# Kernel optimization log

Measured on AMD Instinct MI355X. Metric: run time of the kernel, lower is better.

Reference implementation:

```python
import jax, jax.numpy as jnp
import numpy as np

B, S, D = 2, 2048, 1024
H = 16
HD = D // H


def setup_inputs() -> dict:
    key = jax.random.key(0)
    ks = jax.random.split(key, 6)
    X = jax.random.normal(ks[0], (B, S, D), dtype=jnp.float32)
    # Linear weights stored [in, out] so y = x @ W (torch stores transposed).
    sc = 1.0 / np.sqrt(D)
    Wq = jax.random.normal(ks[1], (D, D), dtype=jnp.float32) * sc
    Wk = jax.random.normal(ks[2], (D, D), dtype=jnp.float32) * sc
    Wv = jax.random.normal(ks[3], (D, D), dtype=jnp.float32) * sc
    Wo = jax.random.normal(ks[4], (D, D), dtype=jnp.float32) * sc
    bo = jax.random.normal(ks[5], (D,), dtype=jnp.float32) * 0.01
    return {"X": X, "Wq": Wq, "Wk": Wk, "Wv": Wv, "Wo": Wo, "bo": bo}


def reference(X, Wq, Wk, Wv, Wo, bo):
    b, n, _ = X.shape
    # QKV projections (no bias, qkv_bias=False), reshape to [b, h, n, hd]
    q = (X @ Wq).reshape(b, n, H, HD).transpose(0, 2, 1, 3)
    k = (X @ Wk).reshape(b, n, H, HD).transpose(0, 2, 1, 3)
    v = (X @ Wv).reshape(b, n, H, HD).transpose(0, 2, 1, 3)
    # Unscaled scores (module's scale flag defaults to False)
    scores = jnp.einsum("bhqd,bhkd->bhqk", q, k)
    causal = jnp.triu(jnp.ones((n, n), dtype=bool), k=1)  # True above diagonal
    scores = jnp.where(causal, -jnp.inf, scores)
    attn = jax.nn.softmax(scores, axis=-1)
    # dropout p=0.0 -> identity
    ctx = jnp.einsum("bhqk,bhkd->bqhd", attn, v).reshape(b, n, H * HD)
    return ctx @ Wo + bo
```

## Files before the change

### kernel.cpp

```cpp
#include <hip/hip_runtime.h>
#include <stdint.h>


typedef __attribute__((ext_vector_type(8))) short short8;
typedef __attribute__((ext_vector_type(4))) float floatx4;

#define S_LEN 2048
#define D_DIM 1024
#define NH 16
#define HD 64
#define L2E 1.44269504088896340736f

__device__ __forceinline__ short f2bf(float f) {
    uint32_t u = __builtin_bit_cast(uint32_t, f);
    uint32_t r = u + 0x7fffu + ((u >> 16) & 1u);
    return (short)(r >> 16);
}
__device__ __forceinline__ uint32_t pack2(float a, float b) {
#if __has_builtin(__builtin_amdgcn_cvt_pk_bf16_f32)
    auto v = __builtin_amdgcn_cvt_pk_bf16_f32(a, b);
    uint32_t r; __builtin_memcpy(&r, &v, sizeof(r)); return r;
#else
    return (uint32_t)(uint16_t)f2bf(a) | ((uint32_t)(uint16_t)f2bf(b) << 16);
#endif
}
__device__ __forceinline__ void gll16(const void* g, void* l) {
    __builtin_amdgcn_global_load_lds(
        (const __attribute__((address_space(1))) void*)g,
        (__attribute__((address_space(3))) void*)l, 16, 0, 0);
}

__global__ __launch_bounds__(256) void prep_kernel(const float* __restrict__ X,
                                                   const float* __restrict__ Wq,
                                                   const float* __restrict__ Wk,
                                                   const float* __restrict__ Wv,
                                                   const float* __restrict__ Wo,
                                                   short* __restrict__ Xb,
                                                   short* __restrict__ WqkvT,
                                                   short* __restrict__ WoT) {
    const int b = blockIdx.x, tid = threadIdx.x;
    if (b < 4096) {
        const int i = b * 256 + tid;
        const float4 v = *(const float4*)(X + (size_t)i * 4);
        uint2 o;
        o.x = pack2(v.x, v.y);
        o.y = pack2(v.z, v.w);
        *(uint2*)(Xb + (size_t)i * 4) = o;
    } else {
        const int b2 = b - 4096;
        const int z = b2 >> 10, w = b2 & 1023;
        const float* W = (z == 0) ? Wq : (z == 1) ? Wk : (z == 2) ? Wv : Wo;
        short* WT = (z < 3) ? (WqkvT + (size_t)z * 1024 * 1024) : WoT;
        __shared__ float tile[32][33];
        const int bx = (w & 31) * 32;
        const int by = (w >> 5) * 32;
        const int tx = tid & 31, ty = tid >> 5;
        for (int i = 0; i < 32; i += 8)
            tile[ty + i][tx] = W[(size_t)(bx + ty + i) * D_DIM + by + tx];
        __syncthreads();
        for (int i = 0; i < 32; i += 8)
            WT[(size_t)(by + ty + i) * D_DIM + bx + tx] = f2bf(tile[tx][ty + i]);
    }
}

__global__ __launch_bounds__(256, 3) void gemm_qkv_kernel(const short* __restrict__ Xb,
                                                          const short* __restrict__ WT,
                                                          short* __restrict__ Qb,
                                                          short* __restrict__ Kb,
                                                          short* __restrict__ Vtb) {
    __shared__ __align__(16) short smem[16384];
    short (*As)[4096] = (short(*)[4096])smem;
    short (*Bs)[4096] = (short(*)[4096])(smem + 8192);
    const int m0 = blockIdx.x * 128, n0 = blockIdx.y * 128;
    const int tid = threadIdx.x, lane = tid & 63, wave = tid >> 6;
    const int ln = lane & 15, quad = lane >> 4;
    const int mw = (wave & 1) * 64, nw = (wave >> 1) * 64;
    floatx4 acc[4][4] = {};

    const int c0 = tid, c1 = 256 + tid;
    const int r0 = c0 >> 2, s0 = (c0 & 3) ^ ((r0 >> 1) & 3);
    const int r1 = c1 >> 2, s1 = (c1 & 3) ^ ((r1 >> 1) & 3);
    const short* A0 = Xb + (size_t)(m0 + r0) * D_DIM + s0 * 8;
    const short* A1 = Xb + (size_t)(m0 + r1) * D_DIM + s1 * 8;
    const short* B0 = WT + (size_t)(n0 + r0) * D_DIM + s0 * 8;
    const short* B1 = WT + (size_t)(n0 + r1) * D_DIM + s1 * 8;

#define QSTAGE(buf, kk)                                    \
    {                                                      \
        const int o = (kk) * 32;                           \
        gll16(A0 + o, &As[buf][c0 * 8]);                   \
        gll16(A1 + o, &As[buf][c1 * 8]);                   \
        gll16(B0 + o, &Bs[buf][c0 * 8]);                   \
        gll16(B1 + o, &Bs[buf][c1 * 8]);                   \
    }

    QSTAGE(0, 0);
    int cur = 0;
    for (int kk = 0; kk < 32; kk++) {
        if (kk + 1 < 32) {
            QSTAGE(cur ^ 1, kk + 1);
            asm volatile("s_waitcnt vmcnt(4)" ::: "memory");
        } else {
            asm volatile("s_waitcnt vmcnt(0)" ::: "memory");
        }
        __builtin_amdgcn_s_barrier();
        __builtin_amdgcn_sched_barrier(0);
        short8 a[4], b[4];
        for (int i = 0; i < 4; i++) {
            const int row = mw + i * 16 + ln;
            a[i] = *(const short8*)(&As[cur][row * 32 + ((quad ^ ((row >> 1) & 3)) * 8)]);
        }
        for (int j = 0; j < 4; j++) {
            const int row = nw + j * 16 + ln;
            b[j] = *(const short8*)(&Bs[cur][row * 32 + ((quad ^ ((row >> 1) & 3)) * 8)]);
        }
        __builtin_amdgcn_s_setprio(1);
        for (int i = 0; i < 4; i++)
            for (int j = 0; j < 4; j++)
                acc[i][j] = __builtin_amdgcn_mfma_f32_16x16x32_bf16(a[i], b[j], acc[i][j], 0, 0, 0);
        __builtin_amdgcn_s_setprio(0);
        __builtin_amdgcn_sched_barrier(0);
        __builtin_amdgcn_s_barrier();
        __builtin_amdgcn_sched_barrier(0);
        cur ^= 1;
    }
#undef QSTAGE

    const int nsel = n0 >> 10;
    if (nsel < 2) {
        const float qs = (nsel == 0) ? L2E : 1.f;
        short* outB = (nsel == 0) ? Qb : Kb;
        for (int i = 0; i < 4; i++)
            for (int j = 0; j < 4; j++)
                for (int r = 0; r < 4; r++) {
                    const int row = m0 + mw + i * 16 + quad * 4 + r;
                    const int col = (n0 & 1023) + nw + j * 16 + ln;
                    const int bb = row >> 11, s = row & (S_LEN - 1);
                    const int h = col >> 6, hd = col & (HD - 1);
                    outB[(((size_t)(bb * NH + h)) * S_LEN + s) * HD + hd] = f2bf(acc[i][j][r] * qs);
                }
    } else {
        for (int i = 0; i < 4; i++)
            for (int j = 0; j < 4; j++) {
                const int feat = nw + j * 16 + ln;
                const int tok  = mw + i * 16 + quad * 4;
                const int t8 = tok >> 3, lo = tok & 7;
                uint2 u;
                u.x = pack2(acc[i][j][0], acc[i][j][1]);
                u.y = pack2(acc[i][j][2], acc[i][j][3]);
                *(uint2*)&smem[feat * 128 + ((t8 ^ (feat & 15)) * 8) + lo] = u;
            }
        __syncthreads();
        const int bb = m0 >> 11, sbase = m0 & (S_LEN - 1);
        for (int c = tid; c < 2048; c += 256) {
            const int feat = c >> 4, t8 = c & 15;
            const short8 v = *(const short8*)&smem[feat * 128 + ((t8 ^ (feat & 15)) * 8)];
            const int col = (n0 & 1023) + feat;
            const int h = col >> 6, hd = col & (HD - 1);
            const int s = sbase + t8 * 8;
            *(short8*)(Vtb + (((size_t)(bb * NH + h)) * HD + hd) * S_LEN + s) = v;
        }
    }
}

__global__ __launch_bounds__(256, 3) void gemm_out_kernel(const short* __restrict__ Cb,
                                                          const short* __restrict__ WoT,
                                                          float* __restrict__ out,
                                                          const float* __restrict__ bias) {
    __shared__ __align__(16) short As[2][128 * 32];
    __shared__ __align__(16) short Bs[2][64 * 32];
    const int m0 = blockIdx.x * 128, n0 = blockIdx.y * 64;
    const int tid = threadIdx.x, lane = tid & 63;
    const int ln = lane & 15, quad = lane >> 4;
    const int wave = tid >> 6;
    const int mw = (wave & 1) * 64, nw = (wave >> 1) * 32;

    floatx4 acc[4][2] = {};

    const int c0 = tid, c1 = 256 + tid;
    const int r0 = c0 >> 2, s0 = (c0 & 3) ^ ((r0 >> 1) & 3);
    const int r1 = c1 >> 2, s1 = (c1 & 3) ^ ((r1 >> 1) & 3);
    const short* A0 = Cb + (size_t)(m0 + r0) * D_DIM + s0 * 8;
    const short* A1 = Cb + (size_t)(m0 + r1) * D_DIM + s1 * 8;
    const short* B0 = WoT + (size_t)(n0 + r0) * D_DIM + s0 * 8;

#define OSTAGE(buf, kk)                                    \
    {                                                      \
        const int o = (kk) * 32;                           \
        gll16(A0 + o, &As[buf][c0 * 8]);                   \
        gll16(A1 + o, &As[buf][c1 * 8]);                   \
        gll16(B0 + o, &Bs[buf][c0 * 8]);                   \
    }

    OSTAGE(0, 0);
    int cur = 0;
    for (int kk = 0; kk < 32; kk++) {
        if (kk + 1 < 32) {
            OSTAGE(cur ^ 1, kk + 1);
            asm volatile("s_waitcnt vmcnt(3)" ::: "memory");
        } else {
            asm volatile("s_waitcnt vmcnt(0)" ::: "memory");
        }
        __builtin_amdgcn_s_barrier();
        __builtin_amdgcn_sched_barrier(0);
        short8 a[4], b[2];
        for (int i = 0; i < 4; i++) {
            const int row = mw + i * 16 + ln;
            a[i] = *(const short8*)(&As[cur][row * 32 + ((quad ^ ((row >> 1) & 3)) * 8)]);
        }
        for (int j = 0; j < 2; j++) {
            const int row = nw + j * 16 + ln;
            b[j] = *(const short8*)(&Bs[cur][row * 32 + ((quad ^ ((row >> 1) & 3)) * 8)]);
        }
        __builtin_amdgcn_s_setprio(1);
        for (int i = 0; i < 4; i++)
            for (int j = 0; j < 2; j++)
                acc[i][j] = __builtin_amdgcn_mfma_f32_16x16x32_bf16(a[i], b[j], acc[i][j], 0, 0, 0);
        __builtin_amdgcn_s_setprio(0);
        __builtin_amdgcn_sched_barrier(0);
        __builtin_amdgcn_s_barrier();
        __builtin_amdgcn_sched_barrier(0);
        cur ^= 1;
    }
#undef OSTAGE

    for (int i = 0; i < 4; i++)
        for (int j = 0; j < 2; j++)
            for (int r = 0; r < 4; r++) {
                const int row = m0 + mw + i * 16 + quad * 4 + r;
                const int col = n0 + nw + j * 16 + ln;
                out[(size_t)row * D_DIM + col] = acc[i][j][r] + bias[col];
            }
}

__global__ __launch_bounds__(512, 6) void attn_kernel(const short* __restrict__ Q,
                                                      const short* __restrict__ Kg,
                                                      const short* __restrict__ Vt,
                                                      short* __restrict__ ctx,
                                                      float* __restrict__ Opart,
                                                      float* __restrict__ Lpart,
                                                      int bh_base) {
    __shared__ __align__(16) short Ks[2][64 * 64];
    __shared__ __align__(16) short Vs[2][64 * 64];
    __shared__ __align__(16) short Ps[8][640];

    const int tid = threadIdx.x, wave = tid >> 6, lane = tid & 63;
    const int ln = lane & 15, quad = lane >> 4;

    const int id = blockIdx.x;
    const int bh = bh_base + (id & 7) + 8 * ((id >> 3) & 1);
    const int t = id >> 4;

    static const unsigned char TASK[24] = {
        0xF0, 0xE1, 0xD0, 0xC1, 0xB0, 0xA1, 0x90, 0x81,
        0xF1, 0xE0, 0xD1, 0xC0, 0xB1, 0xA0, 0x91, 0x80,
        0x02, 0x12, 0x22, 0x32, 0x42, 0x52, 0x62, 0x72};
    const int code = TASK[t];
    const int qt = code >> 4, mode = code & 3;
    const int n = qt + 1, h0 = n >> 1;
    const int kb = 2 * ((mode == 1) ? h0 : 0);
    const int ke = 2 * ((mode == 0) ? h0 : n);
    const int pidx   = (mode == 2) ? -1 : ((qt - 8) * 32 + bh) * 2 + mode;
    const int kmask0 = 2 * qt;
    const int q0 = qt * 128;
    const int bb = bh >> 4, h = bh & 15;
    short* Pw = Ps[wave];

    const short* qrow = Q + ((size_t)bh * S_LEN + q0 + wave * 16 + ln) * HD;
    const short8 qb0 = *(const short8*)(qrow + quad * 8);
    const short8 qb1 = *(const short8*)(qrow + 32 + quad * 8);
    const int q_abs = q0 + wave * 16 + ln;

    const int srow = tid >> 3, spos = tid & 7, ssrc = spos ^ (srow & 7);
    const size_t kbase = (size_t)bh * S_LEN * HD;
    const size_t vbase = (size_t)bh * HD * S_LEN;

    float l_part = 0.f;
    floatx4 o_acc[4] = {};

#define STAGE(buf, kt_)                                                          \
    {                                                                            \
        const int k0s = (kt_) * 64;                                              \
        gll16(Kg + kbase + (size_t)(k0s + srow) * HD + ssrc * 8,                 \
              &Ks[buf][tid * 8]);                                                \
        gll16(Vt + vbase + (size_t)srow * S_LEN + k0s + ssrc * 8,                \
              &Vs[buf][tid * 8]);                                                \
    }

    int cur = 0;
    STAGE(0, kb);
    for (int kt = kb; kt < ke; kt++) {
        if (kt + 1 < ke) {
            STAGE(cur ^ 1, kt + 1);
            asm volatile("s_waitcnt vmcnt(2)" ::: "memory");
        } else {
            asm volatile("s_waitcnt vmcnt(0)" ::: "memory");
        }
        __builtin_amdgcn_s_barrier();
        __builtin_amdgcn_sched_barrier(0);

        const short* Kc = Ks[cur];
        const short* Vc = Vs[cur];

        floatx4 sc4[4];
        __builtin_amdgcn_s_setprio(1);
        for (int nt = 0; nt < 4; nt++) {
            const int row = nt * 16 + ln;
            const short8 ak0 = *(const short8*)(Kc + row * 64 + ((quad ^ (ln & 7)) * 8));
            const short8 ak1 = *(const short8*)(Kc + row * 64 + (((4 + quad) ^ (ln & 7)) * 8));
            floatx4 z = {};
            z = __builtin_amdgcn_mfma_f32_16x16x32_bf16(ak0, qb0, z, 0, 0, 0);
            z = __builtin_amdgcn_mfma_f32_16x16x32_bf16(ak1, qb1, z, 0, 0, 0);
            sc4[nt] = z;
        }
        __builtin_amdgcn_s_setprio(0);

        if (kt >= kmask0) {
            const int k0 = kt * 64;
            for (int nt = 0; nt < 4; nt++)
                for (int r = 0; r < 4; r++)
                    if (k0 + nt * 16 + quad * 4 + r > q_abs) sc4[nt][r] = -1e30f;
        }

        float ls = 0.f;
        for (int nt = 0; nt < 4; nt++)
            for (int r = 0; r < 4; r++) {
                const float e = exp2f(sc4[nt][r]);
                sc4[nt][r] = e; ls += e;
            }
        l_part += ls;

        for (int p = 0; p < 2; p++) {
            uint2 u0, u1;
            u0.x = pack2(sc4[2 * p][0], sc4[2 * p][1]);
            u0.y = pack2(sc4[2 * p][2], sc4[2 * p][3]);
            u1.x = pack2(sc4[2 * p + 1][0], sc4[2 * p + 1][1]);
            u1.y = pack2(sc4[2 * p + 1][2], sc4[2 * p + 1][3]);
            *(uint2*)&Pw[ln * 40 + quad * 4]      = u0;
            *(uint2*)&Pw[ln * 40 + 16 + quad * 4] = u1;
            const short8 bp = *(const short8*)&Pw[ln * 40 + quad * 8];
            __builtin_amdgcn_s_setprio(1);
            for (int dt = 0; dt < 4; dt++) {
                const int row = dt * 16 + ln;
                const short8 av = *(const short8*)(Vc + row * 64 + (((p * 4 + quad) ^ (ln & 7)) * 8));
                o_acc[dt] = __builtin_amdgcn_mfma_f32_16x16x32_bf16(av, bp, o_acc[dt], 0, 0, 0);
            }
            __builtin_amdgcn_s_setprio(0);
        }

        __builtin_amdgcn_sched_barrier(0);
        __builtin_amdgcn_s_barrier();
        __builtin_amdgcn_sched_barrier(0);
        cur ^= 1;
    }
#undef STAGE

    float l_tot = l_part;
    l_tot += __shfl_xor(l_tot, 16, 64);
    l_tot += __shfl_xor(l_tot, 32, 64);

    if (pidx >= 0) {
        float* Ob = Opart + (size_t)pidx * 8192 + (wave * 16 + ln) * 64;
        for (int dt = 0; dt < 4; dt++)
            *(float4*)(Ob + dt * 16 + quad * 4) = *(float4*)&o_acc[dt];
        if (quad == 0) Lpart[(size_t)pidx * 128 + wave * 16 + ln] = l_tot;
    } else {
        const float rl = 1.f / l_tot;
        const int qr = lane >> 2, sg = lane & 3;
        for (int c = 0; c < 2; c++) {
            for (int dd = 0; dd < 2; dd++) {
                const int dt = c * 2 + dd;
                uint2 u;
                u.x = pack2(o_acc[dt][0] * rl, o_acc[dt][1] * rl);
                u.y = pack2(o_acc[dt][2] * rl, o_acc[dt][3] * rl);
                *(uint2*)&Pw[ln * 40 + dd * 16 + quad * 4] = u;
            }
            const short8 v = *(const short8*)&Pw[qr * 40 + sg * 8];
            const int s = q0 + wave * 16 + qr;
            *(short8*)(ctx + ((size_t)bb * S_LEN + s) * D_DIM + h * HD + sg * 8 + c * 32) = v;
        }
    }
}

__global__ __launch_bounds__(256) void combine_kernel(const float* __restrict__ Opart,
                                                      const float* __restrict__ Lpart,
                                                      short* __restrict__ ctx) {
    const int tile = blockIdx.x;
    const int qt = 8 + (tile >> 5), bh = tile & 31;
    const int bb = bh >> 4, h = bh & 15;
    const int p0 = ((qt - 8) * 32 + bh) * 2;
    const float* O0 = Opart + (size_t)p0 * 8192;
    const float* O1 = O0 + 8192;
    const float* l0 = Lpart + (size_t)p0 * 128;
    const float* l1 = l0 + 128;
    for (int e = threadIdx.x; e < 2048; e += 256) {
        const int q = e >> 4, seg = e & 15;
        const float rl = 1.f / (l0[q] + l1[q]);
        const float4 x0 = *(const float4*)(O0 + q * 64 + seg * 4);
        const float4 x1 = *(const float4*)(O1 + q * 64 + seg * 4);
        uint2 u;
        u.x = pack2((x0.x + x1.x) * rl, (x0.y + x1.y) * rl);
        u.y = pack2((x0.z + x1.z) * rl, (x0.w + x1.w) * rl);
        const int s = qt * 128 + q;
        *(uint2*)(ctx + ((size_t)bb * S_LEN + s) * D_DIM + h * HD + seg * 4) = u;
    }
}

extern "C" void kernel_launch(void* const* d_in, const int* in_sizes, int n_in,
                              void* d_out, int out_size, void* d_ws, size_t ws_size,
                              hipStream_t stream) {
    const float* X  = (const float*)d_in[0];
    const float* Wq = (const float*)d_in[1];
    const float* Wk = (const float*)d_in[2];
    const float* Wv = (const float*)d_in[3];
    const float* Wo = (const float*)d_in[4];
    const float* bo = (const float*)d_in[5];
    float* out = (float*)d_out;

    char* ws = (char*)d_ws;
    const size_t MB = 1024 * 1024;
    short* Xb     = (short*)(ws);
    short* WqkvT  = (short*)(ws + 8  * MB);
    short* Qb     = (short*)(ws + 16 * MB);
    short* Kb     = (short*)(ws + 24 * MB);
    short* Vtb    = (short*)(ws + 32 * MB);
    short* ctxb   = (short*)(ws + 40 * MB);
    short* WoT    = (short*)(ws + 48 * MB);
    float* Opart  = (float*)(ws);
    float* Lpart  = (float*)(ws + 50 * MB);

    prep_kernel<<<8192, 256, 0, stream>>>(X, Wq, Wk, Wv, Wo, Xb, WqkvT, WoT);

    dim3 gq(32, 24);
    gemm_qkv_kernel<<<gq, 256, 0, stream>>>(Xb, WqkvT, Qb, Kb, Vtb);

    attn_kernel<<<384, 512, 0, stream>>>(Qb, Kb, Vtb, ctxb, Opart, Lpart, 0);
    attn_kernel<<<384, 512, 0, stream>>>(Qb, Kb, Vtb, ctxb, Opart, Lpart, 16);
    combine_kernel<<<256, 256, 0, stream>>>(Opart, Lpart, ctxb);

    dim3 go(32, 16);
    gemm_out_kernel<<<go, 256, 0, stream>>>(ctxb, WoT, out, bo);
}
```

Baseline: 204.8 us.

## Drop split-K attention and combine kernel; use 128-wide KV tiles in one launch

Replaces the two split-KV attention launches and the fp32 partial-combine kernel with a single launch of 512 blocks. Each block handles one query tile over its full causal KV range and orders blocks longest-first to balance load. KV tiles grow from 64 to 128 keys, halving the loop iterations and barriers, at the cost of twice the LDS, more registers and a lower occupancy hint (6 to 4). It also removes the partial-result global traffic and one kernel launch, but long query tiles can no longer be split across blocks, so the tail may be less balanced.

Result: faster. 178.8 us (-12.7%).

```diff
diff --git a/kernel.cpp b/kernel.cpp
--- a/kernel.cpp
+++ b/kernel.cpp
@@ -233,35 +233,22 @@
             }
 }
 
-__global__ __launch_bounds__(512, 6) void attn_kernel(const short* __restrict__ Q,
+__global__ __launch_bounds__(512, 4) void attn_kernel(const short* __restrict__ Q,
                                                       const short* __restrict__ Kg,
                                                       const short* __restrict__ Vt,
-                                                      short* __restrict__ ctx,
-                                                      float* __restrict__ Opart,
-                                                      float* __restrict__ Lpart,
-                                                      int bh_base) {
-    __shared__ __align__(16) short Ks[2][64 * 64];
-    __shared__ __align__(16) short Vs[2][64 * 64];
+                                                      short* __restrict__ ctx) {
+    __shared__ __align__(16) short Ks[2][128 * 64];
+    __shared__ __align__(16) short Vs[2][64 * 128];
     __shared__ __align__(16) short Ps[8][640];
 
     const int tid = threadIdx.x, wave = tid >> 6, lane = tid & 63;
     const int ln = lane & 15, quad = lane >> 4;
 
     const int id = blockIdx.x;
-    const int bh = bh_base + (id & 7) + 8 * ((id >> 3) & 1);
-    const int t = id >> 4;
-
-    static const unsigned char TASK[24] = {
-        0xF0, 0xE1, 0xD0, 0xC1, 0xB0, 0xA1, 0x90, 0x81,
-        0xF1, 0xE0, 0xD1, 0xC0, 0xB1, 0xA0, 0x91, 0x80,
-        0x02, 0x12, 0x22, 0x32, 0x42, 0x52, 0x62, 0x72};
-    const int code = TASK[t];
-    const int qt = code >> 4, mode = code & 3;
-    const int n = qt + 1, h0 = n >> 1;
-    const int kb = 2 * ((mode == 1) ? h0 : 0);
-    const int ke = 2 * ((mode == 0) ? h0 : n);
-    const int pidx   = (mode == 2) ? -1 : ((qt - 8) * 32 + bh) * 2 + mode;
-    const int kmask0 = 2 * qt;
+    const int hv = (id < 256) ? id : id - 256;
+    const int bh = (hv & 7) + 8 * ((hv >> 3) & 3);
+    const int qt = (id < 256) ? 8 + (hv >> 5) : 7 - (hv >> 5);
+    const int ke = qt + 1;
     const int q0 = qt * 128;
     const int bb = bh >> 4, h = bh & 15;
     short* Pw = Ps[wave];
@@ -271,28 +258,32 @@
     const short8 qb1 = *(const short8*)(qrow + 32 + quad * 8);
     const int q_abs = q0 + wave * 16 + ln;
 
-    const int srow = tid >> 3, spos = tid & 7, ssrc = spos ^ (srow & 7);
     const size_t kbase = (size_t)bh * S_LEN * HD;
     const size_t vbase = (size_t)bh * HD * S_LEN;
+    const int ck0 = tid, ck1 = tid + 512;
+    const int kr0 = ck0 >> 3, ks0 = (ck0 & 7) ^ (kr0 & 7);
+    const int kr1 = ck1 >> 3, ks1 = (ck1 & 7) ^ (kr1 & 7);
+    const int vr0 = ck0 >> 4, vs0 = (ck0 & 15) ^ (vr0 & 15);
+    const int vr1 = ck1 >> 4, vs1 = (ck1 & 15) ^ (vr1 & 15);
 
     float l_part = 0.f;
     floatx4 o_acc[4] = {};
 
-#define STAGE(buf, kt_)                                                          \
-    {                                                                            \
-        const int k0s = (kt_) * 64;                                              \
-        gll16(Kg + kbase + (size_t)(k0s + srow) * HD + ssrc * 8,                 \
-              &Ks[buf][tid * 8]);                                                \
-        gll16(Vt + vbase + (size_t)srow * S_LEN + k0s + ssrc * 8,                \
-              &Vs[buf][tid * 8]);                                                \
+#define STAGE(buf, kt_)                                                           \
+    {                                                                             \
+        const int k0s = (kt_) * 128;                                              \
+        gll16(Kg + kbase + (size_t)(k0s + kr0) * HD + ks0 * 8, &Ks[buf][ck0 * 8]);\
+        gll16(Kg + kbase + (size_t)(k0s + kr1) * HD + ks1 * 8, &Ks[buf][ck1 * 8]);\
+        gll16(Vt + vbase + (size_t)vr0 * S_LEN + k0s + vs0 * 8, &Vs[buf][ck0 * 8]);\
+        gll16(Vt + vbase + (size_t)vr1 * S_LEN + k0s + vs1 * 8, &Vs[buf][ck1 * 8]);\
     }
 
     int cur = 0;
-    STAGE(0, kb);
-    for (int kt = kb; kt < ke; kt++) {
+    STAGE(0, 0);
+    for (int kt = 0; kt < ke; kt++) {
         if (kt + 1 < ke) {
             STAGE(cur ^ 1, kt + 1);
-            asm volatile("s_waitcnt vmcnt(2)" ::: "memory");
+            asm volatile("s_waitcnt vmcnt(4)" ::: "memory");
         } else {
             asm volatile("s_waitcnt vmcnt(0)" ::: "memory");
         }
@@ -302,47 +293,47 @@
         const short* Kc = Ks[cur];
         const short* Vc = Vs[cur];
 
-        floatx4 sc4[4];
+        floatx4 sc[8];
         __builtin_amdgcn_s_setprio(1);
-        for (int nt = 0; nt < 4; nt++) {
+        for (int nt = 0; nt < 8; nt++) {
             const int row = nt * 16 + ln;
             const short8 ak0 = *(const short8*)(Kc + row * 64 + ((quad ^ (ln & 7)) * 8));
             const short8 ak1 = *(const short8*)(Kc + row * 64 + (((4 + quad) ^ (ln & 7)) * 8));
             floatx4 z = {};
             z = __builtin_amdgcn_mfma_f32_16x16x32_bf16(ak0, qb0, z, 0, 0, 0);
             z = __builtin_amdgcn_mfma_f32_16x16x32_bf16(ak1, qb1, z, 0, 0, 0);
-            sc4[nt] = z;
+            sc[nt] = z;
         }
         __builtin_amdgcn_s_setprio(0);
 
-        if (kt >= kmask0) {
-            const int k0 = kt * 64;
-            for (int nt = 0; nt < 4; nt++)
+        if (kt == qt) {
+            const int k0 = kt * 128;
+            for (int nt = 0; nt < 8; nt++)
                 for (int r = 0; r < 4; r++)
-                    if (k0 + nt * 16 + quad * 4 + r > q_abs) sc4[nt][r] = -1e30f;
+                    if (k0 + nt * 16 + quad * 4 + r > q_abs) sc[nt][r] = -1e30f;
         }
 
         float ls = 0.f;
-        for (int nt = 0; nt < 4; nt++)
+        for (int nt = 0; nt < 8; nt++)
             for (int r = 0; r < 4; r++) {
-                const float e = exp2f(sc4[nt][r]);
-                sc4[nt][r] = e; ls += e;
+                const float e = exp2f(sc[nt][r]);
+                sc[nt][r] = e; ls += e;
             }
         l_part += ls;
 
-        for (int p = 0; p < 2; p++) {
+        for (int p = 0; p < 4; p++) {
             uint2 u0, u1;
-            u0.x = pack2(sc4[2 * p][0], sc4[2 * p][1]);
-            u0.y = pack2(sc4[2 * p][2], sc4[2 * p][3]);
-            u1.x = pack2(sc4[2 * p + 1][0], sc4[2 * p + 1][1]);
-            u1.y = pack2(sc4[2 * p + 1][2], sc4[2 * p + 1][3]);
+            u0.x = pack2(sc[2 * p][0], sc[2 * p][1]);
+            u0.y = pack2(sc[2 * p][2], sc[2 * p][3]);
+            u1.x = pack2(sc[2 * p + 1][0], sc[2 * p + 1][1]);
+            u1.y = pack2(sc[2 * p + 1][2], sc[2 * p + 1][3]);
             *(uint2*)&Pw[ln * 40 + quad * 4]      = u0;
             *(uint2*)&Pw[ln * 40 + 16 + quad * 4] = u1;
             const short8 bp = *(const short8*)&Pw[ln * 40 + quad * 8];
             __builtin_amdgcn_s_setprio(1);
             for (int dt = 0; dt < 4; dt++) {
                 const int row = dt * 16 + ln;
-                const short8 av = *(const short8*)(Vc + row * 64 + (((p * 4 + quad) ^ (ln & 7)) * 8));
+                const short8 av = *(const short8*)(Vc + row * 128 + (((p * 4 + quad) ^ (ln & 15)) * 8));
                 o_acc[dt] = __builtin_amdgcn_mfma_f32_16x16x32_bf16(av, bp, o_acc[dt], 0, 0, 0);
             }
             __builtin_amdgcn_s_setprio(0);
@@ -359,50 +350,19 @@
     l_tot += __shfl_xor(l_tot, 16, 64);
     l_tot += __shfl_xor(l_tot, 32, 64);
 
-    if (pidx >= 0) {
-        float* Ob = Opart + (size_t)pidx * 8192 + (wave * 16 + ln) * 64;
-        for (int dt = 0; dt < 4; dt++)
-            *(float4*)(Ob + dt * 16 + quad * 4) = *(float4*)&o_acc[dt];
-        if (quad == 0) Lpart[(size_t)pidx * 128 + wave * 16 + ln] = l_tot;
-    } else {
-        const float rl = 1.f / l_tot;
-        const int qr = lane >> 2, sg = lane & 3;
-        for (int c = 0; c < 2; c++) {
-            for (int dd = 0; dd < 2; dd++) {
-                const int dt = c * 2 + dd;
-                uint2 u;
-                u.x = pack2(o_acc[dt][0] * rl, o_acc[dt][1] * rl);
-                u.y = pack2(o_acc[dt][2] * rl, o_acc[dt][3] * rl);
-                *(uint2*)&Pw[ln * 40 + dd * 16 + quad * 4] = u;
-            }
-            const short8 v = *(const short8*)&Pw[qr * 40 + sg * 8];
-            const int s = q0 + wave * 16 + qr;
-            *(short8*)(ctx + ((size_t)bb * S_LEN + s) * D_DIM + h * HD + sg * 8 + c * 32) = v;
-        }
-    }
-}
-
-__global__ __launch_bounds__(256) void combine_kernel(const float* __restrict__ Opart,
-                                                      const float* __restrict__ Lpart,
-                                                      short* __restrict__ ctx) {
-    const int tile = blockIdx.x;
-    const int qt = 8 + (tile >> 5), bh = tile & 31;
-    const int bb = bh >> 4, h = bh & 15;
-    const int p0 = ((qt - 8) * 32 + bh) * 2;
-    const float* O0 = Opart + (size_t)p0 * 8192;
-    const float* O1 = O0 + 8192;
-    const float* l0 = Lpart + (size_t)p0 * 128;
-    const float* l1 = l0 + 128;
-    for (int e = threadIdx.x; e < 2048; e += 256) {
-        const int q = e >> 4, seg = e & 15;
-        const float rl = 1.f / (l0[q] + l1[q]);
-        const float4 x0 = *(const float4*)(O0 + q * 64 + seg * 4);
-        const float4 x1 = *(const float4*)(O1 + q * 64 + seg * 4);
-        uint2 u;
-        u.x = pack2((x0.x + x1.x) * rl, (x0.y + x1.y) * rl);
-        u.y = pack2((x0.z + x1.z) * rl, (x0.w + x1.w) * rl);
-        const int s = qt * 128 + q;
-        *(uint2*)(ctx + ((size_t)bb * S_LEN + s) * D_DIM + h * HD + seg * 4) = u;
+    const float rl = 1.f / l_tot;
+    const int qr = lane >> 2, sg = lane & 3;
+    for (int c = 0; c < 2; c++) {
+        for (int dd = 0; dd < 2; dd++) {
+            const int dt = c * 2 + dd;
+            uint2 u;
+            u.x = pack2(o_acc[dt][0] * rl, o_acc[dt][1] * rl);
+            u.y = pack2(o_acc[dt][2] * rl, o_acc[dt][3] * rl);
+            *(uint2*)&Pw[ln * 40 + dd * 16 + quad * 4] = u;
+        }
+        const short8 v = *(const short8*)&Pw[qr * 40 + sg * 8];
+        const int s = q0 + wave * 16 + qr;
+        *(short8*)(ctx + ((size_t)bb * S_LEN + s) * D_DIM + h * HD + sg * 8 + c * 32) = v;
     }
 }
 
@@ -426,17 +386,13 @@
     short* Vtb    = (short*)(ws + 32 * MB);
     short* ctxb   = (short*)(ws + 40 * MB);
     short* WoT    = (short*)(ws + 48 * MB);
-    float* Opart  = (float*)(ws);
-    float* Lpart  = (float*)(ws + 50 * MB);
 
     prep_kernel<<<8192, 256, 0, stream>>>(X, Wq, Wk, Wv, Wo, Xb, WqkvT, WoT);
 
     dim3 gq(32, 24);
     gemm_qkv_kernel<<<gq, 256, 0, stream>>>(Xb, WqkvT, Qb, Kb, Vtb);
 
-    attn_kernel<<<384, 512, 0, stream>>>(Qb, Kb, Vtb, ctxb, Opart, Lpart, 0);
-    attn_kernel<<<384, 512, 0, stream>>>(Qb, Kb, Vtb, ctxb, Opart, Lpart, 16);
-    combine_kernel<<<256, 256, 0, stream>>>(Opart, Lpart, ctxb);
+    attn_kernel<<<512, 512, 0, stream>>>(Qb, Kb, Vtb, ctxb);
 
     dim3 go(32, 16);
     gemm_out_kernel<<<go, 256, 0, stream>>>(ctxb, WoT, out, bo);
```

## Replace split-KV static attention schedule with persistent atomic work queue

Applied to the files above, without the earlier changes.

Removes the static split-KV task table, the partial-output buffers and the combine kernel. One persistent attention launch now pulls (q-tile, head) tasks in longest-first order from a global atomic counter, which prep_kernel resets. This drops a launch and the partial-sum round trip through memory, and balances the causal triangle's uneven work dynamically. In exchange, each long q-tile is done by a single block with no KV split, and every task pays for an atomic fetch plus an extra barrier.

Result: no change. 203.3 us (-0.8%).

```diff
diff --git a/kernel.cpp b/kernel.cpp
--- a/kernel.cpp
+++ b/kernel.cpp
@@ -37,9 +37,11 @@
                                                    const float* __restrict__ Wo,
                                                    short* __restrict__ Xb,
                                                    short* __restrict__ WqkvT,
-                                                   short* __restrict__ WoT) {
+                                                   short* __restrict__ WoT,
+                                                   int* __restrict__ ctr) {
     const int b = blockIdx.x, tid = threadIdx.x;
     if (b < 4096) {
+        if (b == 0 && tid == 0) ctr[0] = 0;
         const int i = b * 256 + tid;
         const float4 v = *(const float4*)(X + (size_t)i * 4);
         uint2 o;
@@ -237,46 +239,42 @@
                                                       const short* __restrict__ Kg,
                                                       const short* __restrict__ Vt,
                                                       short* __restrict__ ctx,
-                                                      float* __restrict__ Opart,
-                                                      float* __restrict__ Lpart,
-                                                      int bh_base) {
+                                                      int* __restrict__ ctr) {
     __shared__ __align__(16) short Ks[2][64 * 64];
     __shared__ __align__(16) short Vs[2][64 * 64];
     __shared__ __align__(16) short Ps[8][640];
+    __shared__ int s_task;
 
     const int tid = threadIdx.x, wave = tid >> 6, lane = tid & 63;
     const int ln = lane & 15, quad = lane >> 4;
-
-    const int id = blockIdx.x;
-    const int bh = bh_base + (id & 7) + 8 * ((id >> 3) & 1);
-    const int t = id >> 4;
-
-    static const unsigned char TASK[24] = {
-        0xF0, 0xE1, 0xD0, 0xC1, 0xB0, 0xA1, 0x90, 0x81,
-        0xF1, 0xE0, 0xD1, 0xC0, 0xB1, 0xA0, 0x91, 0x80,
-        0x02, 0x12, 0x22, 0x32, 0x42, 0x52, 0x62, 0x72};
-    const int code = TASK[t];
-    const int qt = code >> 4, mode = code & 3;
-    const int n = qt + 1, h0 = n >> 1;
-    const int kb = 2 * ((mode == 1) ? h0 : 0);
-    const int ke = 2 * ((mode == 0) ? h0 : n);
-    const int pidx   = (mode == 2) ? -1 : ((qt - 8) * 32 + bh) * 2 + mode;
-    const int kmask0 = 2 * qt;
-    const int q0 = qt * 128;
-    const int bb = bh >> 4, h = bh & 15;
     short* Pw = Ps[wave];
 
-    const short* qrow = Q + ((size_t)bh * S_LEN + q0 + wave * 16 + ln) * HD;
-    const short8 qb0 = *(const short8*)(qrow + quad * 8);
-    const short8 qb1 = *(const short8*)(qrow + 32 + quad * 8);
-    const int q_abs = q0 + wave * 16 + ln;
-
     const int srow = tid >> 3, spos = tid & 7, ssrc = spos ^ (srow & 7);
-    const size_t kbase = (size_t)bh * S_LEN * HD;
-    const size_t vbase = (size_t)bh * HD * S_LEN;
-
-    float l_part = 0.f;
-    floatx4 o_acc[4] = {};
+
+    for (;;) {
+        if (tid == 0) s_task = atomicAdd(ctr, 1);
+        __syncthreads();
+        const int t = s_task;
+        if (t >= 512) return;
+
+        const int qt = 15 - (t >> 5);
+        const int hv = t & 31;
+        const int bh = (hv & 7) + 8 * ((hv >> 3) & 3);
+        const int ke = 2 * (qt + 1);
+        const int kmask0 = 2 * qt;
+        const int q0 = qt * 128;
+        const int bb = bh >> 4, h = bh & 15;
+
+        const short* qrow = Q + ((size_t)bh * S_LEN + q0 + wave * 16 + ln) * HD;
+        const short8 qb0 = *(const short8*)(qrow + quad * 8);
+        const short8 qb1 = *(const short8*)(qrow + 32 + quad * 8);
+        const int q_abs = q0 + wave * 16 + ln;
+
+        const size_t kbase = (size_t)bh * S_LEN * HD;
+        const size_t vbase = (size_t)bh * HD * S_LEN;
+
+        float l_part = 0.f;
+        floatx4 o_acc[4] = {};
 
 #define STAGE(buf, kt_)                                                          \
     {                                                                            \
@@ -287,84 +285,78 @@
               &Vs[buf][tid * 8]);                                                \
     }
 
-    int cur = 0;
-    STAGE(0, kb);
-    for (int kt = kb; kt < ke; kt++) {
-        if (kt + 1 < ke) {
-            STAGE(cur ^ 1, kt + 1);
-            asm volatile("s_waitcnt vmcnt(2)" ::: "memory");
-        } else {
-            asm volatile("s_waitcnt vmcnt(0)" ::: "memory");
-        }
-        __builtin_amdgcn_s_barrier();
-        __builtin_amdgcn_sched_barrier(0);
-
-        const short* Kc = Ks[cur];
-        const short* Vc = Vs[cur];
-
-        floatx4 sc4[4];
-        __builtin_amdgcn_s_setprio(1);
-        for (int nt = 0; nt < 4; nt++) {
-            const int row = nt * 16 + ln;
-            const short8 ak0 = *(const short8*)(Kc + row * 64 + ((quad ^ (ln & 7)) * 8));
-            const short8 ak1 = *(const short8*)(Kc + row * 64 + (((4 + quad) ^ (ln & 7)) * 8));
-            floatx4 z = {};
-            z = __builtin_amdgcn_mfma_f32_16x16x32_bf16(ak0, qb0, z, 0, 0, 0);
-            z = __builtin_amdgcn_mfma_f32_16x16x32_bf16(ak1, qb1, z, 0, 0, 0);
-            sc4[nt] = z;
-        }
-        __builtin_amdgcn_s_setprio(0);
-
-        if (kt >= kmask0) {
-            const int k0 = kt * 64;
+        int cur = 0;
+        STAGE(0, 0);
+        for (int kt = 0; kt < ke; kt++) {
+            if (kt + 1 < ke) {
+                STAGE(cur ^ 1, kt + 1);
+                asm volatile("s_waitcnt vmcnt(2)" ::: "memory");
+            } else {
+                asm volatile("s_waitcnt vmcnt(0)" ::: "memory");
+            }
+            __builtin_amdgcn_s_barrier();
+            __builtin_amdgcn_sched_barrier(0);
+
+            const short* Kc = Ks[cur];
+            const short* Vc = Vs[cur];
+
+            floatx4 sc4[4];
+            __builtin_amdgcn_s_setprio(1);
+            for (int nt = 0; nt < 4; nt++) {
+                const int row = nt * 16 + ln;
+                const short8 ak0 = *(const short8*)(Kc + row * 64 + ((quad ^ (ln & 7)) * 8));
+                const short8 ak1 = *(const short8*)(Kc + row * 64 + (((4 + quad) ^ (ln & 7)) * 8));
+                floatx4 z = {};
+                z = __builtin_amdgcn_mfma_f32_16x16x32_bf16(ak0, qb0, z, 0, 0, 0);
+                z = __builtin_amdgcn_mfma_f32_16x16x32_bf16(ak1, qb1, z, 0, 0, 0);
+                sc4[nt] = z;
+            }
+            __builtin_amdgcn_s_setprio(0);
+
+            if (kt >= kmask0) {
+                const int k0 = kt * 64;
+                for (int nt = 0; nt < 4; nt++)
+                    for (int r = 0; r < 4; r++)
+                        if (k0 + nt * 16 + quad * 4 + r > q_abs) sc4[nt][r] = -1e30f;
+            }
+
+            float ls = 0.f;
             for (int nt = 0; nt < 4; nt++)
-                for (int r = 0; r < 4; r++)
-                    if (k0 + nt * 16 + quad * 4 + r > q_abs) sc4[nt][r] = -1e30f;
-        }
-
-        float ls = 0.f;
-        for (int nt = 0; nt < 4; nt++)
-            for (int r = 0; r < 4; r++) {
-                const float e = exp2f(sc4[nt][r]);
-                sc4[nt][r] = e; ls += e;
-            }
-        l_part += ls;
-
-        for (int p = 0; p < 2; p++) {
-            uint2 u0, u1;
-            u0.x = pack2(sc4[2 * p][0], sc4[2 * p][1]);
-            u0.y = pack2(sc4[2 * p][2], sc4[2 * p][3]);
-            u1.x = pack2(sc4[2 * p + 1][0], sc4[2 * p + 1][1]);
-            u1.y = pack2(sc4[2 * p + 1][2], sc4[2 * p + 1][3]);
-            *(uint2*)&Pw[ln * 40 + quad * 4]      = u0;
-            *(uint2*)&Pw[ln * 40 + 16 + quad * 4] = u1;
-            const short8 bp = *(const short8*)&Pw[ln * 40 + quad * 8];
-            __builtin_amdgcn_s_setprio(1);
-            for (int dt = 0; dt < 4; dt++) {
-                const int row = dt * 16 + ln;
-                const short8 av = *(const short8*)(Vc + row * 64 + (((p * 4 + quad) ^ (ln & 7)) * 8));
-                o_acc[dt] = __builtin_amdgcn_mfma_f32_16x16x32_bf16(av, bp, o_acc[dt], 0, 0, 0);
-            }
-            __builtin_amdgcn_s_setprio(0);
-        }
-
-        __builtin_amdgcn_sched_barrier(0);
-        __builtin_amdgcn_s_barrier();
-        __builtin_amdgcn_sched_barrier(0);
-        cur ^= 1;
-    }
+                for (int r = 0; r < 4; r++) {
+                    const float e = exp2f(sc4[nt][r]);
+                    sc4[nt][r] = e; ls += e;
+                }
+            l_part += ls;
+
+            for (int p = 0; p < 2; p++) {
+                uint2 u0, u1;
+                u0.x = pack2(sc4[2 * p][0], sc4[2 * p][1]);
+                u0.y = pack2(sc4[2 * p][2], sc4[2 * p][3]);
+                u1.x = pack2(sc4[2 * p + 1][0], sc4[2 * p + 1][1]);
+                u1.y = pack2(sc4[2 * p + 1][2], sc4[2 * p + 1][3]);
+                *(uint2*)&Pw[ln * 40 + quad * 4]      = u0;
+                *(uint2*)&Pw[ln * 40 + 16 + quad * 4] = u1;
+                const short8 bp = *(const short8*)&Pw[ln * 40 + quad * 8];
+                __builtin_amdgcn_s_setprio(1);
+                for (int dt = 0; dt < 4; dt++) {
+                    const int row = dt * 16 + ln;
+                    const short8 av = *(const short8*)(Vc + row * 64 + (((p * 4 + quad) ^ (ln & 7)) * 8));
+                    o_acc[dt] = __builtin_amdgcn_mfma_f32_16x16x32_bf16(av, bp, o_acc[dt], 0, 0, 0);
+                }
+                __builtin_amdgcn_s_setprio(0);
+            }
+
+            __builtin_amdgcn_sched_barrier(0);
+            __builtin_amdgcn_s_barrier();
+            __builtin_amdgcn_sched_barrier(0);
+            cur ^= 1;
+        }
 #undef STAGE
 
-    float l_tot = l_part;
-    l_tot += __shfl_xor(l_tot, 16, 64);
-    l_tot += __shfl_xor(l_tot, 32, 64);
-
-    if (pidx >= 0) {
-        float* Ob = Opart + (size_t)pidx * 8192 + (wave * 16 + ln) * 64;
-        for (int dt = 0; dt < 4; dt++)
-            *(float4*)(Ob + dt * 16 + quad * 4) = *(float4*)&o_acc[dt];
-        if (quad == 0) Lpart[(size_t)pidx * 128 + wave * 16 + ln] = l_tot;
-    } else {
+        float l_tot = l_part;
+        l_tot += __shfl_xor(l_tot, 16, 64);
+        l_tot += __shfl_xor(l_tot, 32, 64);
+
         const float rl = 1.f / l_tot;
         const int qr = lane >> 2, sg = lane & 3;
         for (int c = 0; c < 2; c++) {
@@ -379,30 +371,7 @@
             const int s = q0 + wave * 16 + qr;
             *(short8*)(ctx + ((size_t)bb * S_LEN + s) * D_DIM + h * HD + sg * 8 + c * 32) = v;
         }
-    }
-}
-
-__global__ __launch_bounds__(256) void combine_kernel(const float* __restrict__ Opart,
-                                                      const float* __restrict__ Lpart,
-                                                      short* __restrict__ ctx) {
-    const int tile = blockIdx.x;
-    const int qt = 8 + (tile >> 5), bh = tile & 31;
-    const int bb = bh >> 4, h = bh & 15;
-    const int p0 = ((qt - 8) * 32 + bh) * 2;
-    const float* O0 = Opart + (size_t)p0 * 8192;
-    const float* O1 = O0 + 8192;
-    const float* l0 = Lpart + (size_t)p0 * 128;
-    const float* l1 = l0 + 128;
-    for (int e = threadIdx.x; e < 2048; e += 256) {
-        const int q = e >> 4, seg = e & 15;
-        const float rl = 1.f / (l0[q] + l1[q]);
-        const float4 x0 = *(const float4*)(O0 + q * 64 + seg * 4);
-        const float4 x1 = *(const float4*)(O1 + q * 64 + seg * 4);
-        uint2 u;
-        u.x = pack2((x0.x + x1.x) * rl, (x0.y + x1.y) * rl);
-        u.y = pack2((x0.z + x1.z) * rl, (x0.w + x1.w) * rl);
-        const int s = qt * 128 + q;
-        *(uint2*)(ctx + ((size_t)bb * S_LEN + s) * D_DIM + h * HD + seg * 4) = u;
+        __syncthreads();
     }
 }
 
@@ -426,17 +395,14 @@
     short* Vtb    = (short*)(ws + 32 * MB);
     short* ctxb   = (short*)(ws + 40 * MB);
     short* WoT    = (short*)(ws + 48 * MB);
-    float* Opart  = (float*)(ws);
-    float* Lpart  = (float*)(ws + 50 * MB);
-
-    prep_kernel<<<8192, 256, 0, stream>>>(X, Wq, Wk, Wv, Wo, Xb, WqkvT, WoT);
+    int*   ctr    = (int*)(ws + 51 * MB);
+
+    prep_kernel<<<8192, 256, 0, stream>>>(X, Wq, Wk, Wv, Wo, Xb, WqkvT, WoT, ctr);
 
     dim3 gq(32, 24);
     gemm_qkv_kernel<<<gq, 256, 0, stream>>>(Xb, WqkvT, Qb, Kb, Vtb);
 
-    attn_kernel<<<384, 512, 0, stream>>>(Qb, Kb, Vtb, ctxb, Opart, Lpart, 0);
-    attn_kernel<<<384, 512, 0, stream>>>(Qb, Kb, Vtb, ctxb, Opart, Lpart, 16);
-    combine_kernel<<<256, 256, 0, stream>>>(Opart, Lpart, ctxb);
+    attn_kernel<<<768, 512, 0, stream>>>(Qb, Kb, Vtb, ctxb, ctr);
 
     dim3 go(32, 16);
     gemm_out_kernel<<<go, 256, 0, stream>>>(ctxb, WoT, out, bo);
```
